# Performance work log

Hardware: AMD Instinct MI355X
Metric: run time of the kernel (lower is better)

The kernel has to match this reference:

```python
import jax, jax.numpy as jnp
import numpy as np

T, B, F = 2048, 2, 1024
H = 16
DK = F // H


def setup_inputs() -> dict:
    key = jax.random.key(0)
    ks = jax.random.split(key, 13)
    s = 0.02
    return {
        "query": jax.random.normal(ks[0], (T, B, F), jnp.float32),
        "key": jax.random.normal(ks[1], (T, B, F), jnp.float32),
        "value": jax.random.normal(ks[2], (T, B, F), jnp.float32),
        "key_padding_mask": jax.random.randint(ks[3], (B, T), 0, 2).astype(bool),
        "Wq": jax.random.normal(ks[4], (F, F), jnp.float32) * s,
        "bq": jnp.zeros((F,), jnp.float32),
        "Wk": jax.random.normal(ks[5], (F, F), jnp.float32) * s,
        "bk": jnp.zeros((F,), jnp.float32),
        "Wv": jax.random.normal(ks[6], (F, F), jnp.float32) * s,
        "bv": jnp.zeros((F,), jnp.float32),
        "Wo": jax.random.normal(ks[7], (F, F), jnp.float32) * s,
        "bo": jnp.zeros((F,), jnp.float32),
    }


def reference(query, key, value, key_padding_mask, Wq, bq, Wk, bk, Wv, bv, Wo, bo):
    # inputs are [T, B, F]; module transposes to batch-major [B, T, F]
    q = jnp.swapaxes(query, 0, 1)
    k = jnp.swapaxes(key, 0, 1)
    v = jnp.swapaxes(value, 0, 1)
    nb = q.shape[0]
    # QKV projections, split into heads: [B, H, T, DK]
    def proj(x, W, b):
        y = x @ W.T + b
        return y.reshape(nb, -1, H, DK).transpose(0, 2, 1, 3)
    qh, kh, vh = proj(q, Wq, bq), proj(k, Wk, bk), proj(v, Wv, bv)
    # scores [B, H, Tq, Tk]
    scores = jnp.einsum("bhqd,bhkd->bhqk", qh, kh) / jnp.sqrt(jnp.float32(DK))
    scores = jnp.where(key_padding_mask[:, None, None, :], -jnp.inf, scores)
    attn = jax.nn.softmax(scores, axis=-1)
    # AV + merge heads + out proj (dropout p=0 -> identity)
    ctx = jnp.einsum("bhqk,bhkd->bhqd", attn, vh)
    ctx = ctx.transpose(0, 2, 1, 3).reshape(nb, -1, H * DK)
    out = ctx @ Wo.T + bo
    return jnp.swapaxes(out, 0, 1)  # back to [T, B, F]
```

## Files before the change

kernel.cpp:

```cpp
#include <hip/hip_runtime.h>
#include <hip/hip_bf16.h>
#include <stdint.h>


typedef __bf16 bf16_t;
typedef __bf16 bf16x4 __attribute__((ext_vector_type(4)));
typedef __bf16 bf16x8 __attribute__((ext_vector_type(8)));
typedef float f32x4 __attribute__((ext_vector_type(4)));
typedef unsigned int u32x2 __attribute__((ext_vector_type(2)));

typedef const __attribute__((address_space(1))) void* gas_ptr;
typedef __attribute__((address_space(3))) void* las_ptr;

__device__ __forceinline__ void gload16(const void* g, void* lds) {
    __builtin_amdgcn_global_load_lds((gas_ptr)g, (las_ptr)lds, 16, 0, 0);
}

__device__ __forceinline__ int swz(int o) { return o ^ (((o >> 7) & 7) << 4); }

__device__ __forceinline__ int gofs(int c) {
    return ((c >> 5) << 9) + (((c >> 1) & 3) << 7) + (((c >> 3) & 3) << 5) + ((c & 1) << 4);
}

#define TRREAD(dst, addr, IMM) \
    asm volatile("ds_read_b64_tr_b16 %0, %1 offset:" #IMM : "=v"(dst) : "v"(addr))

#if __has_builtin(__builtin_amdgcn_exp2f)
#define EXP2F(x) __builtin_amdgcn_exp2f(x)
#else
#define EXP2F(x) exp2f(x)
#endif
#if __has_builtin(__builtin_amdgcn_rcpf)
#define RCPF(x) __builtin_amdgcn_rcpf(x)
#else
#define RCPF(x) (1.0f / (x))
#endif

__global__ __launch_bounds__(256) void prep_all_kernel(const float* __restrict__ q,
                                                       const float* __restrict__ k,
                                                       const float* __restrict__ v,
                                                       const float* __restrict__ wq,
                                                       const float* __restrict__ wk,
                                                       const float* __restrict__ wv,
                                                       const float* __restrict__ wo,
                                                       const unsigned char* __restrict__ mraw,
                                                       bf16_t* __restrict__ xdst,
                                                       bf16_t* __restrict__ wdst,
                                                       unsigned long long* __restrict__ mbits) {
    const int bidx = blockIdx.x;
    const int tid = threadIdx.x;
    if (bidx < 6144) {
        int idx = bidx * 256 + tid;
        int which = idx >> 19;
        int loc = idx & 524287;
        const float* src = which == 0 ? q : which == 1 ? k : v;
        int e0 = loc * 8;
        int t = e0 >> 11, r = e0 & 2047, b = r >> 10, f = r & 1023;
        const float4* s = (const float4*)(src + e0);
        float4 a = s[0], c = s[1];
        bf16x8 o;
        o[0] = (bf16_t)a.x; o[1] = (bf16_t)a.y; o[2] = (bf16_t)a.z; o[3] = (bf16_t)a.w;
        o[4] = (bf16_t)c.x; o[5] = (bf16_t)c.y; o[6] = (bf16_t)c.z; o[7] = (bf16_t)c.w;
        *(bf16x8*)(xdst + (size_t)which * 4194304 + ((size_t)b * 2048 + t) * 1024 + f) = o;
    } else if (bidx < 8192) {
        int idx = (bidx - 6144) * 256 + tid;
        int which = idx >> 17;
        int loc = idx & 131071;
        const float* src = which == 0 ? wq : which == 1 ? wk : which == 2 ? wv : wo;
        int e0 = loc * 8;
        const float4* s = (const float4*)(src + e0);
        float4 a = s[0], c = s[1];
        bf16x8 o;
        o[0] = (bf16_t)a.x; o[1] = (bf16_t)a.y; o[2] = (bf16_t)a.z; o[3] = (bf16_t)a.w;
        o[4] = (bf16_t)c.x; o[5] = (bf16_t)c.y; o[6] = (bf16_t)c.z; o[7] = (bf16_t)c.w;
        *(bf16x8*)(wdst + (size_t)which * 1048576 + e0) = o;
    } else {
        __shared__ int s_isbyte;
        if (tid == 0) s_isbyte = 0;
        __syncthreads();
        int any = 0;
        for (int i = tid; i < 4096; i += 256)
            if ((i & 3) && mraw[i]) any = 1;
        if (any) atomicOr(&s_isbyte, 1);
        __syncthreads();
        if (tid < 64) {
            int b = tid >> 5, kt = tid & 31;
            unsigned long long bits = 0;
            if (s_isbyte) {
                for (int j = 0; j < 64; ++j)
                    if (mraw[b * 2048 + kt * 64 + j]) bits |= 1ull << j;
            } else {
                const int* ri = (const int*)mraw;
                for (int j = 0; j < 64; ++j)
                    if (ri[b * 2048 + kt * 64 + j]) bits |= 1ull << j;
            }
            mbits[tid] = bits;
        }
    }
}

__global__ __launch_bounds__(256) void gemm_kernel(const bf16_t* __restrict__ A0,
                                                   const bf16_t* __restrict__ Bw0,
                                                   const float* __restrict__ b0,
                                                   const float* __restrict__ b1,
                                                   const float* __restrict__ b2,
                                                   const unsigned long long* __restrict__ mbits,
                                                   bf16_t* __restrict__ outb,
                                                   float* __restrict__ outf,
                                                   int mode) {
    __shared__ __align__(16) bf16_t Asm[128 * 32];
    __shared__ __align__(16) bf16_t Bsm[128 * 32];
    const int tid = threadIdx.x;
    const int wave = tid >> 6, lane = tid & 63;
    const int g = lane >> 4, lr = lane & 15;
    const int z = blockIdx.z;
    const bf16_t* A  = A0 + (size_t)z * 4194304;
    const bf16_t* Bw = Bw0 + (size_t)z * 1048576;
    const float* bias = z == 0 ? b0 : z == 1 ? b1 : b2;
    const float qsc = (mode == 0 && z == 0) ? 0.18033688f : 1.0f;
    const int m0 = blockIdx.y * 128, n0 = blockIdx.x * 128;
    const int wm = (wave >> 1) * 64, wn = (wave & 1) * 64;
    const int srow = wave * 32 + (lane >> 2);
    const int scol = (lane & 3) * 8;

    f32x4 acc[4][4] = {};

    for (int k0 = 0; k0 < 1024; k0 += 32) {
        __syncthreads();
        gload16(A  + (size_t)(m0 + srow) * 1024 + k0 + scol,      (char*)Asm + wave * 2048);
        gload16(A  + (size_t)(m0 + srow + 16) * 1024 + k0 + scol, (char*)Asm + wave * 2048 + 1024);
        gload16(Bw + (size_t)(n0 + srow) * 1024 + k0 + scol,      (char*)Bsm + wave * 2048);
        gload16(Bw + (size_t)(n0 + srow + 16) * 1024 + k0 + scol, (char*)Bsm + wave * 2048 + 1024);
        __syncthreads();

        bf16x8 af[4], bfr[4];
        #pragma unroll
        for (int mi = 0; mi < 4; ++mi)
            af[mi] = *(const bf16x8*)(Asm + (wm + mi * 16 + lr) * 32 + g * 8);
        #pragma unroll
        for (int ni = 0; ni < 4; ++ni)
            bfr[ni] = *(const bf16x8*)(Bsm + (wn + ni * 16 + lr) * 32 + g * 8);
        #pragma unroll
        for (int mi = 0; mi < 4; ++mi)
            #pragma unroll
            for (int ni = 0; ni < 4; ++ni)
                acc[mi][ni] = __builtin_amdgcn_mfma_f32_16x16x32_bf16(af[mi], bfr[ni], acc[mi][ni], 0, 0, 0);
    }

    #pragma unroll
    for (int mi = 0; mi < 4; ++mi) {
        #pragma unroll
        for (int ni = 0; ni < 4; ++ni) {
            int n = n0 + wn + ni * 16 + lr;
            float bs = bias[n];
            #pragma unroll
            for (int i = 0; i < 4; ++i) {
                int m = m0 + wm + mi * 16 + 4 * g + i;
                float v = (acc[mi][ni][i] + bs) * qsc;
                int b = m >> 11, t = m & 2047;
                if (mode == 0) {
                    if (z != 0) {
                        const bool mk = (mbits[b * 32 + (t >> 6)] >> (t & 63)) & 1;
                        if (mk) v = 0.f;
                    }
                    int hh = n >> 6, dk = n & 63;
                    outb[(size_t)z * 4194304 + ((size_t)(b * 16 + hh) * 2048 + t) * 64 + dk] = (bf16_t)v;
                } else {
                    outf[(size_t)t * 2048 + b * 1024 + n] = v;
                }
            }
        }
    }
}

__global__ __launch_bounds__(256, 2) void attn_kernel(const bf16_t* __restrict__ qh,
                                                      const bf16_t* __restrict__ kh,
                                                      const bf16_t* __restrict__ vh,
                                                      const unsigned long long* __restrict__ mbits,
                                                      bf16_t* __restrict__ ctx) {
    __shared__ __align__(16) bf16_t Ks[2][2][64 * 64];
    __shared__ __align__(16) bf16_t Vs[2][2][64 * 64];

    const int tid = threadIdx.x;
    const int wave = tid >> 6, lane = tid & 63;
    const int g = lane >> 4, lr = lane & 15;
    const int bid = blockIdx.x;
    const int sid = (bid & 7) * 64 + (bid >> 3);
    const int bh = sid >> 4, qc = sid & 15;
    const int b = bh >> 4, h = bh & 15;
    const int q0 = qc * 128;
    const bf16_t* Qg = qh + ((size_t)bh * 2048 + q0) * 64;
    const bf16_t* Kg = kh + (size_t)bh * 2048 * 64;
    const bf16_t* Vg = vh + (size_t)bh * 2048 * 64;
    const unsigned long long* mbp = mbits + b * 32;

    const int dstw = wave * 2048;
    const int dl = dstw + lane * 16;
    const int wq0 = wave * 32;
    const int vs0 = gofs(wave * 128 + lane);
    const int vs1 = gofs(wave * 128 + 64 + lane);

    #pragma unroll
    for (int c = 0; c < 4; ++c)
        gload16((const char*)Qg + swz(wave * 4096 + c * 1024 + lane * 16),
                (char*)Ks[0] + wave * 4096 + c * 1024);
    __syncthreads();
    bf16x8 qf[2][2];
    #pragma unroll
    for (int s = 0; s < 2; ++s) {
        qf[s][0] = *(const bf16x8*)((const char*)Ks[0] + swz((wq0 + s * 16 + lr) * 128 + g * 16));
        qf[s][1] = *(const bf16x8*)((const char*)Ks[0] + swz((wq0 + s * 16 + lr) * 128 + 64 + g * 16));
    }
    __syncthreads();

    #pragma unroll
    for (int u = 0; u < 2; ++u) {
        const char* Kt = (const char*)(Kg + u * 4096);
        const char* Vt = (const char*)(Vg + u * 4096);
        gload16(Kt + swz(dl),        (char*)Ks[0][u] + dstw);
        gload16(Kt + swz(dl + 1024), (char*)Ks[0][u] + dstw + 1024);
        gload16(Vt + vs0,            (char*)Vs[0][u] + dstw);
        gload16(Vt + vs1,            (char*)Vs[0][u] + dstw + 1024);
    }

    bf16x8 ones;
    #pragma unroll
    for (int j = 0; j < 8; ++j) ones[j] = (bf16_t)1.0f;

    f32x4 cacc[2][4] = {};
    f32x4 sacc[2] = {};
    const unsigned vbase = (unsigned)(unsigned long long)(las_ptr)&Vs[0][0][0] + g * 512 + lr * 8;

    for (int m = 0; m < 16; ++m) {
        const int par = m & 1;
        __syncthreads();

        if (m < 15) {
            #pragma unroll
            for (int u = 0; u < 2; ++u) {
                const char* Kn = (const char*)(Kg + (2 * m + 2 + u) * 4096);
                const char* Vn = (const char*)(Vg + (2 * m + 2 + u) * 4096);
                gload16(Kn + swz(dl),        (char*)Ks[par ^ 1][u] + dstw);
                gload16(Kn + swz(dl + 1024), (char*)Ks[par ^ 1][u] + dstw + 1024);
                gload16(Vn + vs0,            (char*)Vs[par ^ 1][u] + dstw);
                gload16(Vn + vs1,            (char*)Vs[par ^ 1][u] + dstw + 1024);
            }
        }

        f32x4 s2[2][2][4];
        __builtin_amdgcn_s_setprio(1);
        #pragma unroll
        for (int u = 0; u < 2; ++u) {
            const char* Kc = (const char*)Ks[par][u];
            #pragma unroll
            for (int st = 0; st < 4; ++st) {
                bf16x8 kf0 = *(const bf16x8*)(Kc + swz((st * 16 + lr) * 128 + g * 16));
                bf16x8 kf1 = *(const bf16x8*)(Kc + swz((st * 16 + lr) * 128 + 64 + g * 16));
                #pragma unroll
                for (int s = 0; s < 2; ++s) {
                    f32x4 zz = {};
                    zz = __builtin_amdgcn_mfma_f32_16x16x32_bf16(kf0, qf[s][0], zz, 0, 0, 0);
                    zz = __builtin_amdgcn_mfma_f32_16x16x32_bf16(kf1, qf[s][1], zz, 0, 0, 0);
                    s2[u][s][st] = zz;
                }
            }
        }
        __builtin_amdgcn_s_setprio(0);

        #pragma unroll
        for (int u = 0; u < 2; ++u) {
            #pragma unroll
            for (int st = 0; st < 4; ++st) {
                #pragma unroll
                for (int i = 0; i < 4; ++i) {
                    s2[u][0][st][i] = EXP2F(s2[u][0][st][i]);
                    s2[u][1][st][i] = EXP2F(s2[u][1][st][i]);
                }
            }
            bf16x8 pb[2][2];
            #pragma unroll
            for (int s = 0; s < 2; ++s)
                #pragma unroll
                for (int kk = 0; kk < 2; ++kk)
                    #pragma unroll
                    for (int j = 0; j < 8; ++j)
                        pb[s][kk][j] = (bf16_t)s2[u][s][2 * kk + (j >> 2)][j & 3];

            const unsigned vb = vbase + (unsigned)par * 16384u + (unsigned)u * 8192u;
            u32x2 t[2][2][4];
            TRREAD(t[0][0][0], vb, 0);    TRREAD(t[0][0][1], vb, 128);
            TRREAD(t[0][0][2], vb, 256);  TRREAD(t[0][0][3], vb, 384);
            TRREAD(t[0][1][0], vb, 2048); TRREAD(t[0][1][1], vb, 2176);
            TRREAD(t[0][1][2], vb, 2304); TRREAD(t[0][1][3], vb, 2432);
            TRREAD(t[1][0][0], vb, 4096); TRREAD(t[1][0][1], vb, 4224);
            TRREAD(t[1][0][2], vb, 4352); TRREAD(t[1][0][3], vb, 4480);
            TRREAD(t[1][1][0], vb, 6144); TRREAD(t[1][1][1], vb, 6272);
            TRREAD(t[1][1][2], vb, 6400); TRREAD(t[1][1][3], vb, 6528);
            asm volatile("s_waitcnt lgkmcnt(0)" ::: "memory");
            __builtin_amdgcn_sched_barrier(0);
            __builtin_amdgcn_s_setprio(1);
            #pragma unroll
            for (int kk = 0; kk < 2; ++kk) {
                sacc[0] = __builtin_amdgcn_mfma_f32_16x16x32_bf16(ones, pb[0][kk], sacc[0], 0, 0, 0);
                sacc[1] = __builtin_amdgcn_mfma_f32_16x16x32_bf16(ones, pb[1][kk], sacc[1], 0, 0, 0);
                #pragma unroll
                for (int ni = 0; ni < 4; ++ni) {
                    union { u32x2 q[2]; bf16x8 v8; } uu;
                    uu.q[0] = t[kk][0][ni];
                    uu.q[1] = t[kk][1][ni];
                    #pragma unroll
                    for (int s = 0; s < 2; ++s)
                        cacc[s][ni] = __builtin_amdgcn_mfma_f32_16x16x32_bf16(uu.v8, pb[s][kk], cacc[s][ni], 0, 0, 0);
                }
            }
            __builtin_amdgcn_s_setprio(0);
        }
    }

    float nm = 0.f;
    #pragma unroll
    for (int i = 0; i < 32; ++i)
        nm += (float)__popcll(mbp[i]);
    #pragma unroll
    for (int s = 0; s < 2; ++s) {
        const float rl = RCPF(sacc[s][0] - nm);
        const int trow = q0 + wq0 + s * 16 + lr;
        #pragma unroll
        for (int ni = 0; ni < 4; ++ni) {
            bf16x4 o;
            #pragma unroll
            for (int i = 0; i < 4; ++i)
                o[i] = (bf16_t)(cacc[s][ni][i] * rl);
            *(bf16x4*)(ctx + ((size_t)b * 2048 + trow) * 1024 + h * 64 + ni * 16 + 4 * g) = o;
        }
    }
}

extern "C" void kernel_launch(void* const* d_in, const int* in_sizes, int n_in,
                              void* d_out, int out_size, void* d_ws, size_t ws_size,
                              hipStream_t stream) {
    const float* query = (const float*)d_in[0];
    const float* key_  = (const float*)d_in[1];
    const float* value = (const float*)d_in[2];
    const unsigned char* kpm_raw = (const unsigned char*)d_in[3];
    const float* Wq = (const float*)d_in[4];
    const float* bq = (const float*)d_in[5];
    const float* Wk = (const float*)d_in[6];
    const float* bk = (const float*)d_in[7];
    const float* Wv = (const float*)d_in[8];
    const float* bv = (const float*)d_in[9];
    const float* Wo = (const float*)d_in[10];
    const float* bo = (const float*)d_in[11];
    float* out = (float*)d_out;

    char* ws = (char*)d_ws;
    size_t off = 0;
    auto alloc = [&](size_t bytes) {
        char* p = ws + off;
        off += (bytes + 255) & ~(size_t)255;
        return p;
    };
    const size_t SZ_X = (size_t)4096 * 1024 * sizeof(bf16_t);
    const size_t SZ_W = (size_t)1024 * 1024 * sizeof(bf16_t);
    bf16_t* xq  = (bf16_t*)alloc(SZ_X);
    bf16_t* xk  = (bf16_t*)alloc(SZ_X);
    bf16_t* xv  = (bf16_t*)alloc(SZ_X);
    bf16_t* wqb = (bf16_t*)alloc(SZ_W);
    bf16_t* wkb = (bf16_t*)alloc(SZ_W);
    bf16_t* wvb = (bf16_t*)alloc(SZ_W);
    bf16_t* wob = (bf16_t*)alloc(SZ_W);
    bf16_t* qhB = (bf16_t*)alloc(SZ_X);
    bf16_t* khB = (bf16_t*)alloc(SZ_X);
    bf16_t* vhB = (bf16_t*)alloc(SZ_X);
    bf16_t* ctxB = (bf16_t*)alloc(SZ_X);
    unsigned long long* mbits = (unsigned long long*)alloc(64 * sizeof(unsigned long long));
    (void)xk; (void)xv; (void)wkb; (void)wvb;

    prep_all_kernel<<<8193, 256, 0, stream>>>(query, key_, value, Wq, Wk, Wv, Wo,
                                              kpm_raw, xq, wqb, mbits);

    gemm_kernel<<<dim3(8, 32, 3), 256, 0, stream>>>(xq, wqb, bq, bk, bv, mbits, qhB, nullptr, 0);

    attn_kernel<<<512, 256, 0, stream>>>(qhB, khB, vhB, mbits, ctxB);

    gemm_kernel<<<dim3(8, 32, 1), 256, 0, stream>>>(ctxB, wob, bo, bo, bo, mbits, nullptr, out, 1);
}
```

Before: 138.6 us.

## Double-buffer GEMM LDS tiles and remap blocks across XCDs

The projection GEMM kernel now keeps two LDS buffers and issues the global-to-LDS loads for the next K slice before computing on the current one, so memory latency can overlap the MFMA work. The launch grid changes from 3D to 1D, and block IDs are remapped so that blocks sharing the same XCD (round-robin by blockIdx mod 8) get contiguous tiles, which is meant to improve L2 reuse of A and B. The cost is double the shared memory per block, which may reduce occupancy, and a correctness dependence on __syncthreads draining outstanding async loads.

```diff
diff --git a/kernel.cpp b/kernel.cpp
--- a/kernel.cpp
+++ b/kernel.cpp
@@ -108,44 +108,56 @@
                                                    bf16_t* __restrict__ outb,
                                                    float* __restrict__ outf,
                                                    int mode) {
-    __shared__ __align__(16) bf16_t Asm[128 * 32];
-    __shared__ __align__(16) bf16_t Bsm[128 * 32];
+    __shared__ __align__(16) bf16_t Asm[2][128 * 32];
+    __shared__ __align__(16) bf16_t Bsm[2][128 * 32];
     const int tid = threadIdx.x;
     const int wave = tid >> 6, lane = tid & 63;
     const int g = lane >> 4, lr = lane & 15;
-    const int z = blockIdx.z;
+
+    const int nb = (mode == 0) ? 768 : 256;
+    const int chunk = nb >> 3;
+    const int sid = (blockIdx.x & 7) * chunk + (blockIdx.x >> 3);
+    const int z = sid >> 8;
+    const int rem = sid & 255;
+    const int m0 = (rem >> 3) * 128, n0 = (rem & 7) * 128;
+
     const bf16_t* A  = A0 + (size_t)z * 4194304;
     const bf16_t* Bw = Bw0 + (size_t)z * 1048576;
     const float* bias = z == 0 ? b0 : z == 1 ? b1 : b2;
     const float qsc = (mode == 0 && z == 0) ? 0.18033688f : 1.0f;
-    const int m0 = blockIdx.y * 128, n0 = blockIdx.x * 128;
     const int wm = (wave >> 1) * 64, wn = (wave & 1) * 64;
     const int srow = wave * 32 + (lane >> 2);
     const int scol = (lane & 3) * 8;
 
+    #define STAGE_GEMM(k0, buf)                                                            \
+        gload16(A  + (size_t)(m0 + srow) * 1024 + (k0) + scol,      (char*)Asm[buf] + wave * 2048);        \
+        gload16(A  + (size_t)(m0 + srow + 16) * 1024 + (k0) + scol, (char*)Asm[buf] + wave * 2048 + 1024); \
+        gload16(Bw + (size_t)(n0 + srow) * 1024 + (k0) + scol,      (char*)Bsm[buf] + wave * 2048);        \
+        gload16(Bw + (size_t)(n0 + srow + 16) * 1024 + (k0) + scol, (char*)Bsm[buf] + wave * 2048 + 1024);
+
+    STAGE_GEMM(0, 0);
+
     f32x4 acc[4][4] = {};
 
-    for (int k0 = 0; k0 < 1024; k0 += 32) {
+    for (int i = 0; i < 32; ++i) {
+        const int cur = i & 1;
         __syncthreads();
-        gload16(A  + (size_t)(m0 + srow) * 1024 + k0 + scol,      (char*)Asm + wave * 2048);
-        gload16(A  + (size_t)(m0 + srow + 16) * 1024 + k0 + scol, (char*)Asm + wave * 2048 + 1024);
-        gload16(Bw + (size_t)(n0 + srow) * 1024 + k0 + scol,      (char*)Bsm + wave * 2048);
-        gload16(Bw + (size_t)(n0 + srow + 16) * 1024 + k0 + scol, (char*)Bsm + wave * 2048 + 1024);
-        __syncthreads();
+        if (i < 31) { STAGE_GEMM((i + 1) * 32, cur ^ 1); }
 
         bf16x8 af[4], bfr[4];
         #pragma unroll
         for (int mi = 0; mi < 4; ++mi)
-            af[mi] = *(const bf16x8*)(Asm + (wm + mi * 16 + lr) * 32 + g * 8);
+            af[mi] = *(const bf16x8*)(Asm[cur] + (wm + mi * 16 + lr) * 32 + g * 8);
         #pragma unroll
         for (int ni = 0; ni < 4; ++ni)
-            bfr[ni] = *(const bf16x8*)(Bsm + (wn + ni * 16 + lr) * 32 + g * 8);
+            bfr[ni] = *(const bf16x8*)(Bsm[cur] + (wn + ni * 16 + lr) * 32 + g * 8);
         #pragma unroll
         for (int mi = 0; mi < 4; ++mi)
             #pragma unroll
             for (int ni = 0; ni < 4; ++ni)
                 acc[mi][ni] = __builtin_amdgcn_mfma_f32_16x16x32_bf16(af[mi], bfr[ni], acc[mi][ni], 0, 0, 0);
     }
+    #undef STAGE_GEMM
 
     #pragma unroll
     for (int mi = 0; mi < 4; ++mi) {
@@ -379,9 +391,9 @@
     prep_all_kernel<<<8193, 256, 0, stream>>>(query, key_, value, Wq, Wk, Wv, Wo,
                                               kpm_raw, xq, wqb, mbits);
 
-    gemm_kernel<<<dim3(8, 32, 3), 256, 0, stream>>>(xq, wqb, bq, bk, bv, mbits, qhB, nullptr, 0);
+    gemm_kernel<<<768, 256, 0, stream>>>(xq, wqb, bq, bk, bv, mbits, qhB, nullptr, 0);
 
     attn_kernel<<<512, 256, 0, stream>>>(qhB, khB, vhB, mbits, ctxB);
 
-    gemm_kernel<<<dim3(8, 32, 1), 256, 0, stream>>>(ctxB, wob, bo, bo, bo, mbits, nullptr, out, 1);
-}
+    gemm_kernel<<<256, 256, 0, stream>>>(ctxB, wob, bo, bo, bo, mbits, nullptr, out, 1);
+}
```

New measurement: 141.5 us. 1.02x slower.

## Fuse fp32-to-bf16 activation conversion and transpose into QKV projection GEMM loads

Applied to the files above, without the earlier changes.

The separate prep pass that converted query/key/value from fp32 to bf16 and transposed them to batch-major is removed. The QKV GEMM now reads fp32 rows directly with transposed indexing, converts in registers and stores the bf16 values to LDS. This drops a full write and re-read of three activation tensors. The grid is also flattened to 1D with a remapped block id that groups tiles per XCD for L2 locality. The cost is fp32 global loads (twice the bytes per tile) through registers instead of direct-to-LDS loads, so that load is not asynchronous.

```diff
diff --git a/kernel.cpp b/kernel.cpp
--- a/kernel.cpp
+++ b/kernel.cpp
@@ -36,34 +36,17 @@
 #define RCPF(x) (1.0f / (x))
 #endif
 
-__global__ __launch_bounds__(256) void prep_all_kernel(const float* __restrict__ q,
-                                                       const float* __restrict__ k,
-                                                       const float* __restrict__ v,
-                                                       const float* __restrict__ wq,
+__global__ __launch_bounds__(256) void prep_all_kernel(const float* __restrict__ wq,
                                                        const float* __restrict__ wk,
                                                        const float* __restrict__ wv,
                                                        const float* __restrict__ wo,
                                                        const unsigned char* __restrict__ mraw,
-                                                       bf16_t* __restrict__ xdst,
                                                        bf16_t* __restrict__ wdst,
                                                        unsigned long long* __restrict__ mbits) {
     const int bidx = blockIdx.x;
     const int tid = threadIdx.x;
-    if (bidx < 6144) {
+    if (bidx < 2048) {
         int idx = bidx * 256 + tid;
-        int which = idx >> 19;
-        int loc = idx & 524287;
-        const float* src = which == 0 ? q : which == 1 ? k : v;
-        int e0 = loc * 8;
-        int t = e0 >> 11, r = e0 & 2047, b = r >> 10, f = r & 1023;
-        const float4* s = (const float4*)(src + e0);
-        float4 a = s[0], c = s[1];
-        bf16x8 o;
-        o[0] = (bf16_t)a.x; o[1] = (bf16_t)a.y; o[2] = (bf16_t)a.z; o[3] = (bf16_t)a.w;
-        o[4] = (bf16_t)c.x; o[5] = (bf16_t)c.y; o[6] = (bf16_t)c.z; o[7] = (bf16_t)c.w;
-        *(bf16x8*)(xdst + (size_t)which * 4194304 + ((size_t)b * 2048 + t) * 1024 + f) = o;
-    } else if (bidx < 8192) {
-        int idx = (bidx - 6144) * 256 + tid;
         int which = idx >> 17;
         int loc = idx & 131071;
         const float* src = which == 0 ? wq : which == 1 ? wk : which == 2 ? wv : wo;
@@ -99,7 +82,10 @@
     }
 }
 
-__global__ __launch_bounds__(256) void gemm_kernel(const bf16_t* __restrict__ A0,
+__global__ __launch_bounds__(256) void gemm_kernel(const float* __restrict__ x0,
+                                                   const float* __restrict__ x1,
+                                                   const float* __restrict__ x2,
+                                                   const bf16_t* __restrict__ Ab,
                                                    const bf16_t* __restrict__ Bw0,
                                                    const float* __restrict__ b0,
                                                    const float* __restrict__ b1,
@@ -113,24 +99,52 @@
     const int tid = threadIdx.x;
     const int wave = tid >> 6, lane = tid & 63;
     const int g = lane >> 4, lr = lane & 15;
-    const int z = blockIdx.z;
-    const bf16_t* A  = A0 + (size_t)z * 4194304;
+
+    const int nb = (mode == 0) ? 768 : 256;
+    const int chunk = nb >> 3;
+    const int sid = (blockIdx.x & 7) * chunk + (blockIdx.x >> 3);
+    const int z = sid >> 8;
+    const int rem = sid & 255;
+    const int m0 = (rem >> 3) * 128, n0 = (rem & 7) * 128;
+
+    const float* Xf = z == 0 ? x0 : z == 1 ? x1 : x2;
     const bf16_t* Bw = Bw0 + (size_t)z * 1048576;
     const float* bias = z == 0 ? b0 : z == 1 ? b1 : b2;
     const float qsc = (mode == 0 && z == 0) ? 0.18033688f : 1.0f;
-    const int m0 = blockIdx.y * 128, n0 = blockIdx.x * 128;
     const int wm = (wave >> 1) * 64, wn = (wave & 1) * 64;
     const int srow = wave * 32 + (lane >> 2);
     const int scol = (lane & 3) * 8;
 
+    const int r0 = m0 + srow, r1 = r0 + 16;
+    const size_t fb0 = (size_t)((r0 & 2047) * 2 + (r0 >> 11)) * 1024 + scol;
+    const size_t fb1 = (size_t)((r1 & 2047) * 2 + (r1 >> 11)) * 1024 + scol;
+    char* dA0 = (char*)Asm + wave * 2048 + lane * 16;
+    char* dA1 = dA0 + 1024;
+
     f32x4 acc[4][4] = {};
 
     for (int k0 = 0; k0 < 1024; k0 += 32) {
         __syncthreads();
-        gload16(A  + (size_t)(m0 + srow) * 1024 + k0 + scol,      (char*)Asm + wave * 2048);
-        gload16(A  + (size_t)(m0 + srow + 16) * 1024 + k0 + scol, (char*)Asm + wave * 2048 + 1024);
-        gload16(Bw + (size_t)(n0 + srow) * 1024 + k0 + scol,      (char*)Bsm + wave * 2048);
-        gload16(Bw + (size_t)(n0 + srow + 16) * 1024 + k0 + scol, (char*)Bsm + wave * 2048 + 1024);
+        if (mode == 0) {
+            float4 a00 = *(const float4*)(Xf + fb0 + k0);
+            float4 a01 = *(const float4*)(Xf + fb0 + k0 + 4);
+            float4 a10 = *(const float4*)(Xf + fb1 + k0);
+            float4 a11 = *(const float4*)(Xf + fb1 + k0 + 4);
+            gload16(Bw + (size_t)(n0 + srow) * 1024 + k0 + scol,      (char*)Bsm + wave * 2048);
+            gload16(Bw + (size_t)(n0 + srow + 16) * 1024 + k0 + scol, (char*)Bsm + wave * 2048 + 1024);
+            bf16x8 w0, w1;
+            w0[0] = (bf16_t)a00.x; w0[1] = (bf16_t)a00.y; w0[2] = (bf16_t)a00.z; w0[3] = (bf16_t)a00.w;
+            w0[4] = (bf16_t)a01.x; w0[5] = (bf16_t)a01.y; w0[6] = (bf16_t)a01.z; w0[7] = (bf16_t)a01.w;
+            w1[0] = (bf16_t)a10.x; w1[1] = (bf16_t)a10.y; w1[2] = (bf16_t)a10.z; w1[3] = (bf16_t)a10.w;
+            w1[4] = (bf16_t)a11.x; w1[5] = (bf16_t)a11.y; w1[6] = (bf16_t)a11.z; w1[7] = (bf16_t)a11.w;
+            *(bf16x8*)dA0 = w0;
+            *(bf16x8*)dA1 = w1;
+        } else {
+            gload16(Ab + (size_t)r0 * 1024 + k0 + scol,               (char*)Asm + wave * 2048);
+            gload16(Ab + (size_t)r1 * 1024 + k0 + scol,               (char*)Asm + wave * 2048 + 1024);
+            gload16(Bw + (size_t)(n0 + srow) * 1024 + k0 + scol,      (char*)Bsm + wave * 2048);
+            gload16(Bw + (size_t)(n0 + srow + 16) * 1024 + k0 + scol, (char*)Bsm + wave * 2048 + 1024);
+        }
         __syncthreads();
 
         bf16x8 af[4], bfr[4];
@@ -362,9 +376,6 @@
     };
     const size_t SZ_X = (size_t)4096 * 1024 * sizeof(bf16_t);
     const size_t SZ_W = (size_t)1024 * 1024 * sizeof(bf16_t);
-    bf16_t* xq  = (bf16_t*)alloc(SZ_X);
-    bf16_t* xk  = (bf16_t*)alloc(SZ_X);
-    bf16_t* xv  = (bf16_t*)alloc(SZ_X);
     bf16_t* wqb = (bf16_t*)alloc(SZ_W);
     bf16_t* wkb = (bf16_t*)alloc(SZ_W);
     bf16_t* wvb = (bf16_t*)alloc(SZ_W);
@@ -374,14 +385,15 @@
     bf16_t* vhB = (bf16_t*)alloc(SZ_X);
     bf16_t* ctxB = (bf16_t*)alloc(SZ_X);
     unsigned long long* mbits = (unsigned long long*)alloc(64 * sizeof(unsigned long long));
-    (void)xk; (void)xv; (void)wkb; (void)wvb;
-
-    prep_all_kernel<<<8193, 256, 0, stream>>>(query, key_, value, Wq, Wk, Wv, Wo,
-                                              kpm_raw, xq, wqb, mbits);
-
-    gemm_kernel<<<dim3(8, 32, 3), 256, 0, stream>>>(xq, wqb, bq, bk, bv, mbits, qhB, nullptr, 0);
+    (void)wkb; (void)wvb;
+
+    prep_all_kernel<<<2049, 256, 0, stream>>>(Wq, Wk, Wv, Wo, kpm_raw, wqb, mbits);
+
+    gemm_kernel<<<768, 256, 0, stream>>>(query, key_, value, nullptr, wqb,
+                                         bq, bk, bv, mbits, qhB, nullptr, 0);
 
     attn_kernel<<<512, 256, 0, stream>>>(qhB, khB, vhB, mbits, ctxB);
 
-    gemm_kernel<<<dim3(8, 32, 1), 256, 0, stream>>>(ctxB, wob, bo, bo, bo, mbits, nullptr, out, 1);
-}
+    gemm_kernel<<<256, 256, 0, stream>>>(nullptr, nullptr, nullptr, ctxB, wob,
+                                         bo, bo, bo, mbits, nullptr, out, 1);
+}
```

New measurement: 128.1 us. -7.5%, faster.

## Triple-buffer GEMM LDS loads with async prefetch and XCD-aware block swizzle

Applied to the files above, without the earlier changes.

Splits the generic GEMM into dedicated QKV and output-projection kernels. Each uses a three-stage LDS ring, issuing async global-to-LDS loads two k-steps ahead and synchronising with vmcnt waits plus a single barrier per step instead of two. Block indices are remapped so consecutive blocks on each XCD share A/B tiles, which should improve L2 reuse. The cost is three times the LDS per block, which may lower occupancy, plus hand-managed waitcnt logic that is fragile.

```diff
diff --git a/kernel.cpp b/kernel.cpp
--- a/kernel.cpp
+++ b/kernel.cpp
@@ -99,53 +99,89 @@
     }
 }
 
-__global__ __launch_bounds__(256) void gemm_kernel(const bf16_t* __restrict__ A0,
-                                                   const bf16_t* __restrict__ Bw0,
-                                                   const float* __restrict__ b0,
-                                                   const float* __restrict__ b1,
-                                                   const float* __restrict__ b2,
-                                                   const unsigned long long* __restrict__ mbits,
-                                                   bf16_t* __restrict__ outb,
-                                                   float* __restrict__ outf,
-                                                   int mode) {
-    __shared__ __align__(16) bf16_t Asm[128 * 32];
-    __shared__ __align__(16) bf16_t Bsm[128 * 32];
+__global__ __launch_bounds__(256) void gemm_qkv_kernel(const bf16_t* __restrict__ A0,
+                                                       const bf16_t* __restrict__ Bw0,
+                                                       const float* __restrict__ b0,
+                                                       const float* __restrict__ b1,
+                                                       const float* __restrict__ b2,
+                                                       const unsigned long long* __restrict__ mbits,
+                                                       bf16_t* __restrict__ outb) {
+    __shared__ __align__(16) bf16_t Asm[3][128 * 32];
+    __shared__ __align__(16) bf16_t Bsm[3][128 * 32];
     const int tid = threadIdx.x;
     const int wave = tid >> 6, lane = tid & 63;
     const int g = lane >> 4, lr = lane & 15;
-    const int z = blockIdx.z;
+
+    const int sid = (blockIdx.x & 7) * 96 + (blockIdx.x >> 3);
+    const int z = sid >> 8;
+    const int rem = sid & 255;
+    const int m0 = (rem >> 3) * 128, n0 = (rem & 7) * 128;
+
     const bf16_t* A  = A0 + (size_t)z * 4194304;
     const bf16_t* Bw = Bw0 + (size_t)z * 1048576;
     const float* bias = z == 0 ? b0 : z == 1 ? b1 : b2;
-    const float qsc = (mode == 0 && z == 0) ? 0.18033688f : 1.0f;
-    const int m0 = blockIdx.y * 128, n0 = blockIdx.x * 128;
+    const float qsc = (z == 0) ? 0.18033688f : 1.0f;
     const int wm = (wave >> 1) * 64, wn = (wave & 1) * 64;
     const int srow = wave * 32 + (lane >> 2);
     const int scol = (lane & 3) * 8;
+    const bf16_t* gA0 = A  + (size_t)(m0 + srow) * 1024 + scol;
+    const bf16_t* gA1 = A  + (size_t)(m0 + srow + 16) * 1024 + scol;
+    const bf16_t* gB0 = Bw + (size_t)(n0 + srow) * 1024 + scol;
+    const bf16_t* gB1 = Bw + (size_t)(n0 + srow + 16) * 1024 + scol;
 
     f32x4 acc[4][4] = {};
 
-    for (int k0 = 0; k0 < 1024; k0 += 32) {
-        __syncthreads();
-        gload16(A  + (size_t)(m0 + srow) * 1024 + k0 + scol,      (char*)Asm + wave * 2048);
-        gload16(A  + (size_t)(m0 + srow + 16) * 1024 + k0 + scol, (char*)Asm + wave * 2048 + 1024);
-        gload16(Bw + (size_t)(n0 + srow) * 1024 + k0 + scol,      (char*)Bsm + wave * 2048);
-        gload16(Bw + (size_t)(n0 + srow + 16) * 1024 + k0 + scol, (char*)Bsm + wave * 2048 + 1024);
-        __syncthreads();
-
-        bf16x8 af[4], bfr[4];
-        #pragma unroll
-        for (int mi = 0; mi < 4; ++mi)
-            af[mi] = *(const bf16x8*)(Asm + (wm + mi * 16 + lr) * 32 + g * 8);
-        #pragma unroll
-        for (int ni = 0; ni < 4; ++ni)
-            bfr[ni] = *(const bf16x8*)(Bsm + (wn + ni * 16 + lr) * 32 + g * 8);
-        #pragma unroll
-        for (int mi = 0; mi < 4; ++mi)
-            #pragma unroll
-            for (int ni = 0; ni < 4; ++ni)
-                acc[mi][ni] = __builtin_amdgcn_mfma_f32_16x16x32_bf16(af[mi], bfr[ni], acc[mi][ni], 0, 0, 0);
-    }
+#define STAGE(t_, bf_) do {                                                   \
+        const int k_ = (t_) * 32;                                             \
+        gload16(gA0 + k_, (char*)Asm[bf_] + wave * 2048);                     \
+        gload16(gA1 + k_, (char*)Asm[bf_] + wave * 2048 + 1024);              \
+        gload16(gB0 + k_, (char*)Bsm[bf_] + wave * 2048);                     \
+        gload16(gB1 + k_, (char*)Bsm[bf_] + wave * 2048 + 1024);              \
+    } while (0)
+
+#define COMPUTE(bf_) do {                                                     \
+        bf16x8 af[4], bfr[4];                                                 \
+        _Pragma("unroll")                                                     \
+        for (int mi = 0; mi < 4; ++mi)                                        \
+            af[mi] = *(const bf16x8*)(Asm[bf_] + (wm + mi * 16 + lr) * 32 + g * 8); \
+        _Pragma("unroll")                                                     \
+        for (int ni = 0; ni < 4; ++ni)                                        \
+            bfr[ni] = *(const bf16x8*)(Bsm[bf_] + (wn + ni * 16 + lr) * 32 + g * 8); \
+        _Pragma("unroll")                                                     \
+        for (int mi = 0; mi < 4; ++mi)                                        \
+            _Pragma("unroll")                                                 \
+            for (int ni = 0; ni < 4; ++ni)                                    \
+                acc[mi][ni] = __builtin_amdgcn_mfma_f32_16x16x32_bf16(af[mi], bfr[ni], acc[mi][ni], 0, 0, 0); \
+    } while (0)
+
+#define BODY(t_, bc_, bs_) do {                                               \
+        asm volatile("s_waitcnt vmcnt(4)" ::: "memory");                      \
+        __builtin_amdgcn_s_barrier();                                         \
+        __builtin_amdgcn_sched_barrier(0);                                    \
+        STAGE((t_) + 2, bs_);                                                 \
+        __builtin_amdgcn_sched_barrier(0);                                    \
+        COMPUTE(bc_);                                                         \
+    } while (0)
+
+    STAGE(0, 0);
+    STAGE(1, 1);
+
+    for (int t = 0; t < 30; t += 3) {
+        BODY(t,     0, 2);
+        BODY(t + 1, 1, 0);
+        BODY(t + 2, 2, 1);
+    }
+    asm volatile("s_waitcnt vmcnt(4)" ::: "memory");
+    __builtin_amdgcn_s_barrier();
+    __builtin_amdgcn_sched_barrier(0);
+    COMPUTE(0);
+    asm volatile("s_waitcnt vmcnt(0)" ::: "memory");
+    __builtin_amdgcn_s_barrier();
+    __builtin_amdgcn_sched_barrier(0);
+    COMPUTE(1);
+#undef BODY
+#undef COMPUTE
+#undef STAGE
 
     #pragma unroll
     for (int mi = 0; mi < 4; ++mi) {
@@ -158,16 +194,101 @@
                 int m = m0 + wm + mi * 16 + 4 * g + i;
                 float v = (acc[mi][ni][i] + bs) * qsc;
                 int b = m >> 11, t = m & 2047;
-                if (mode == 0) {
-                    if (z != 0) {
-                        const bool mk = (mbits[b * 32 + (t >> 6)] >> (t & 63)) & 1;
-                        if (mk) v = 0.f;
-                    }
-                    int hh = n >> 6, dk = n & 63;
-                    outb[(size_t)z * 4194304 + ((size_t)(b * 16 + hh) * 2048 + t) * 64 + dk] = (bf16_t)v;
-                } else {
-                    outf[(size_t)t * 2048 + b * 1024 + n] = v;
+                if (z != 0) {
+                    const bool mk = (mbits[b * 32 + (t >> 6)] >> (t & 63)) & 1;
+                    if (mk) v = 0.f;
                 }
+                int hh = n >> 6, dk = n & 63;
+                outb[(size_t)z * 4194304 + ((size_t)(b * 16 + hh) * 2048 + t) * 64 + dk] = (bf16_t)v;
+            }
+        }
+    }
+}
+
+__global__ __launch_bounds__(256) void gemm_out_kernel(const bf16_t* __restrict__ Ab,
+                                                       const bf16_t* __restrict__ Bw,
+                                                       const float* __restrict__ bias,
+                                                       float* __restrict__ outf) {
+    __shared__ __align__(16) bf16_t Asm[3][128 * 32];
+    __shared__ __align__(16) bf16_t Bsm[3][128 * 32];
+    const int tid = threadIdx.x;
+    const int wave = tid >> 6, lane = tid & 63;
+    const int g = lane >> 4, lr = lane & 15;
+
+    const int sid = (blockIdx.x & 7) * 32 + (blockIdx.x >> 3);
+    const int m0 = (sid >> 3) * 128, n0 = (sid & 7) * 128;
+    const int wm = (wave >> 1) * 64, wn = (wave & 1) * 64;
+    const int srow = wave * 32 + (lane >> 2);
+    const int scol = (lane & 3) * 8;
+    const bf16_t* gA0 = Ab + (size_t)(m0 + srow) * 1024 + scol;
+    const bf16_t* gA1 = Ab + (size_t)(m0 + srow + 16) * 1024 + scol;
+    const bf16_t* gB0 = Bw + (size_t)(n0 + srow) * 1024 + scol;
+    const bf16_t* gB1 = Bw + (size_t)(n0 + srow + 16) * 1024 + scol;
+
+    f32x4 acc[4][4] = {};
+
+#define STAGE(t_, bf_) do {                                                   \
+        const int k_ = (t_) * 32;                                             \
+        gload16(gA0 + k_, (char*)Asm[bf_] + wave * 2048);                     \
+        gload16(gA1 + k_, (char*)Asm[bf_] + wave * 2048 + 1024);              \
+        gload16(gB0 + k_, (char*)Bsm[bf_] + wave * 2048);                     \
+        gload16(gB1 + k_, (char*)Bsm[bf_] + wave * 2048 + 1024);              \
+    } while (0)
+
+#define COMPUTE(bf_) do {                                                     \
+        bf16x8 af[4], bfr[4];                                                 \
+        _Pragma("unroll")                                                     \
+        for (int mi = 0; mi < 4; ++mi)                                        \
+            af[mi] = *(const bf16x8*)(Asm[bf_] + (wm + mi * 16 + lr) * 32 + g * 8); \
+        _Pragma("unroll")                                                     \
+        for (int ni = 0; ni < 4; ++ni)                                        \
+            bfr[ni] = *(const bf16x8*)(Bsm[bf_] + (wn + ni * 16 + lr) * 32 + g * 8); \
+        _Pragma("unroll")                                                     \
+        for (int mi = 0; mi < 4; ++mi)                                        \
+            _Pragma("unroll")                                                 \
+            for (int ni = 0; ni < 4; ++ni)                                    \
+                acc[mi][ni] = __builtin_amdgcn_mfma_f32_16x16x32_bf16(af[mi], bfr[ni], acc[mi][ni], 0, 0, 0); \
+    } while (0)
+
+#define BODY(t_, bc_, bs_) do {                                               \
+        asm volatile("s_waitcnt vmcnt(4)" ::: "memory");                      \
+        __builtin_amdgcn_s_barrier();                                         \
+        __builtin_amdgcn_sched_barrier(0);                                    \
+        STAGE((t_) + 2, bs_);                                                 \
+        __builtin_amdgcn_sched_barrier(0);                                    \
+        COMPUTE(bc_);                                                         \
+    } while (0)
+
+    STAGE(0, 0);
+    STAGE(1, 1);
+    for (int t = 0; t < 30; t += 3) {
+        BODY(t,     0, 2);
+        BODY(t + 1, 1, 0);
+        BODY(t + 2, 2, 1);
+    }
+    asm volatile("s_waitcnt vmcnt(4)" ::: "memory");
+    __builtin_amdgcn_s_barrier();
+    __builtin_amdgcn_sched_barrier(0);
+    COMPUTE(0);
+    asm volatile("s_waitcnt vmcnt(0)" ::: "memory");
+    __builtin_amdgcn_s_barrier();
+    __builtin_amdgcn_sched_barrier(0);
+    COMPUTE(1);
+#undef BODY
+#undef COMPUTE
+#undef STAGE
+
+    #pragma unroll
+    for (int mi = 0; mi < 4; ++mi) {
+        #pragma unroll
+        for (int ni = 0; ni < 4; ++ni) {
+            int n = n0 + wn + ni * 16 + lr;
+            float bs = bias[n];
+            #pragma unroll
+            for (int i = 0; i < 4; ++i) {
+                int m = m0 + wm + mi * 16 + 4 * g + i;
+                int b = m >> 11, t = m & 2047;
+                outf[(size_t)t * 2048 + b * 1024 + n] = acc[mi][ni][i] + bs;
             }
         }
     }
@@ -379,9 +500,9 @@
     prep_all_kernel<<<8193, 256, 0, stream>>>(query, key_, value, Wq, Wk, Wv, Wo,
                                               kpm_raw, xq, wqb, mbits);
 
-    gemm_kernel<<<dim3(8, 32, 3), 256, 0, stream>>>(xq, wqb, bq, bk, bv, mbits, qhB, nullptr, 0);
+    gemm_qkv_kernel<<<768, 256, 0, stream>>>(xq, wqb, bq, bk, bv, mbits, qhB);
 
     attn_kernel<<<512, 256, 0, stream>>>(qhB, khB, vhB, mbits, ctxB);
 
-    gemm_kernel<<<dim3(8, 32, 1), 256, 0, stream>>>(ctxB, wob, bo, bo, bo, mbits, nullptr, out, 1);
-}
+    gemm_out_kernel<<<256, 256, 0, stream>>>(ctxB, wob, bo, out);
+}
```

After: 142.1 us. 2.5% more time.
